# Kernel tuning notes

Measured on AMD Instinct MI355X. Metric: run time of the kernel, lower is better.

Reference implementation:

```python
import jax, jax.numpy as jnp
import numpy as np

B, S, D, H = 2, 2048, 1024, 16
HD = D // H  # head_dim = 64
ROPE_BASE = 10000.0
NEG_MIN = jnp.finfo(jnp.float32).min


def _rope_cos_sin(seq_len, head_dim):
    inv_freq = 1.0 / (ROPE_BASE ** (jnp.arange(0, head_dim, 2, dtype=jnp.float32) / head_dim))
    t = jnp.arange(seq_len, dtype=jnp.float32)
    freqs = jnp.einsum('i,j->ij', t, inv_freq)           # [S, HD/2]
    emb = jnp.concatenate([freqs, freqs], axis=-1)        # [S, HD]
    return jnp.cos(emb), jnp.sin(emb)


def _rotate_half(x):
    x1, x2 = jnp.split(x, 2, axis=-1)
    return jnp.concatenate([-x2, x1], axis=-1)


def setup_inputs() -> dict:
    key = jax.random.key(0)
    ks = jax.random.split(key, 5)
    sc = 0.02
    hidden_states = jax.random.normal(ks[0], (B, S, D), dtype=jnp.float32)
    wq = jax.random.normal(ks[1], (D, D), dtype=jnp.float32) * sc
    wk = jax.random.normal(ks[2], (D, D), dtype=jnp.float32) * sc
    wv = jax.random.normal(ks[3], (D, D), dtype=jnp.float32) * sc
    wo = jax.random.normal(ks[4], (D, D), dtype=jnp.float32) * sc
    # additive causal mask [B,1,S,S]: 0 on/below diagonal, large negative above
    causal = jnp.tril(jnp.ones((S, S), dtype=jnp.bool_))
    attention_mask = jnp.where(causal, 0.0, NEG_MIN)[None, None, :, :].astype(jnp.float32)
    attention_mask = jnp.broadcast_to(attention_mask, (B, 1, S, S))
    position_ids = jnp.broadcast_to(jnp.arange(S, dtype=jnp.int32)[None, :], (B, S))
    return {"hidden_states": hidden_states, "attention_mask": attention_mask,
            "wq": wq, "wk": wk, "wv": wv, "wo": wo, "position_ids": position_ids}


def reference(hidden_states, attention_mask, wq, wk, wv, wo, position_ids):
    bsz, q_len, _ = hidden_states.shape

    def shape_heads(x):
        return x.reshape(bsz, q_len, H, HD).transpose(0, 2, 1, 3)  # [B,H,S,HD]

    q = shape_heads(hidden_states @ wq)
    k = shape_heads(hidden_states @ wk)
    v = shape_heads(hidden_states @ wv)

    cos, sin = _rope_cos_sin(q_len, HD)                   # [S, HD]
    cos = cos[position_ids][:, None, :, :]                # [B,1,S,HD]
    sin = sin[position_ids][:, None, :, :]
    q = q * cos + _rotate_half(q) * sin
    k = k * cos + _rotate_half(k) * sin

    scores = jnp.einsum('bhqd,bhkd->bhqk', q, k) / jnp.sqrt(jnp.float32(HD))
    scores = jnp.maximum(scores + attention_mask, NEG_MIN)
    attn = jax.nn.softmax(scores, axis=-1)
    out = jnp.einsum('bhqk,bhkd->bhqd', attn, v)          # [B,H,S,HD]
    out = out.transpose(0, 2, 1, 3).reshape(bsz, q_len, D)
    return out @ wo
```

## Files before the change

kernel.cpp:

```cpp
#include <hip/hip_runtime.h>
#include <hip/hip_bf16.h>

#define B_ 2
#define S_ 2048
#define D_ 1024
#define H_ 16
#define HD_ 64

typedef unsigned short u16;
typedef __attribute__((ext_vector_type(8))) short short8;
typedef __attribute__((ext_vector_type(4))) float f32x4;

#if __has_builtin(__builtin_amdgcn_exp2f)
#define EXP2F(x) __builtin_amdgcn_exp2f(x)
#else
#define EXP2F(x) exp2f(x)
#endif

__device__ __forceinline__ u16 f2bf(float f) {
  union { float f; unsigned u; } v; v.f = f;
  unsigned r = v.u + 0x7fffu + ((v.u >> 16) & 1u);
  return (u16)(r >> 16);
}
__device__ __forceinline__ unsigned pkbf(float a, float b) {
  union { __hip_bfloat162 h; unsigned u; } v;
  v.h = __float22bfloat162_rn(float2{a, b});
  return v.u;
}
__device__ __forceinline__ void gload_lds16(const u16* g, u16* l) {
  __builtin_amdgcn_global_load_lds((const __attribute__((address_space(1))) void*)g,
                                   (__attribute__((address_space(3))) void*)l, 16, 0, 0);
}

__global__ __launch_bounds__(256) void prep_kernel(const float* __restrict__ hs,
                                                   const float* __restrict__ W0,
                                                   const float* __restrict__ W1,
                                                   const float* __restrict__ W2,
                                                   const float* __restrict__ W3,
                                                   u16* __restrict__ Xb,
                                                   u16* __restrict__ WT) {
  __shared__ float T[64][65];
  if (blockIdx.z == 4) {
    const int base = (blockIdx.y * 16 + blockIdx.x) * 4096 + threadIdx.x;
#pragma unroll 4
    for (int i = 0; i < 16; ++i) {
      const int idx = base + i * 256;
      const float4 v = ((const float4*)hs)[idx];
      ushort4 o;
      o.x = f2bf(v.x); o.y = f2bf(v.y); o.z = f2bf(v.z); o.w = f2bf(v.w);
      ((ushort4*)Xb)[idx] = o;
    }
    return;
  }
  const float* Wz[4] = {W0, W1, W2, W3};
  const float* W = Wz[blockIdx.z];
  u16* dst = WT + (size_t)blockIdx.z * (1024 * 1024);
  const int nb = blockIdx.x * 64, kb = blockIdx.y * 64;
  const int t = threadIdx.x;
  const int r = t >> 2, c4 = (t & 3) * 16;
#pragma unroll
  for (int i = 0; i < 4; ++i) {
    float4 v = *(const float4*)&W[(kb + r) * D_ + nb + c4 + i * 4];
    T[r][c4 + i * 4 + 0] = v.x;
    T[r][c4 + i * 4 + 1] = v.y;
    T[r][c4 + i * 4 + 2] = v.z;
    T[r][c4 + i * 4 + 3] = v.w;
  }
  __syncthreads();
#pragma unroll
  for (int i = 0; i < 4; ++i) {
    ushort4 o;
    o.x = f2bf(T[c4 + i * 4 + 0][r]);
    o.y = f2bf(T[c4 + i * 4 + 1][r]);
    o.z = f2bf(T[c4 + i * 4 + 2][r]);
    o.w = f2bf(T[c4 + i * 4 + 3][r]);
    *(ushort4*)&dst[(nb + r) * D_ + kb + c4 + i * 4] = o;
  }
}

template <int BN, int MODE, int DB>
__global__ __launch_bounds__(256) void gemm_kernel(const u16* __restrict__ A,
                                                   const u16* __restrict__ BT,
                                                   float* __restrict__ out0,
                                                   u16* __restrict__ oQ,
                                                   u16* __restrict__ oK,
                                                   u16* __restrict__ oV,
                                                   const int* __restrict__ posarr) {
  constexpr int K = D_;
  constexpr int NT = BN / 32;
  constexpr int BI = BN / 32;
  constexpr int ABANK = 128 * 64;
  constexpr int BBANK = BN * 64;
  constexpr int STAGE = (DB + 1) * (ABANK + BBANK);
  constexpr int EPIU = (MODE == 1) ? 128 * 136 : 0;
  constexpr int SMU = STAGE > EPIU ? STAGE : EPIU;
  __shared__ u16 smem[SMU];
  u16* AsP = smem;
  u16* BsP = smem + (DB + 1) * ABANK;

  const int t = threadIdx.x, lane = t & 63, w = t >> 6;
  const int l15 = lane & 15, quad = lane >> 4;
  const int n0 = blockIdx.x * BN, m0 = blockIdx.y * 128;
  const int wm = (w >> 1) * 64, wn = (w & 1) * (BN / 2);

  f32x4 acc[4][NT];
#pragma unroll
  for (int mt = 0; mt < 4; ++mt)
#pragma unroll
    for (int nt = 0; nt < NT; ++nt) acc[mt][nt] = (f32x4){0.f, 0.f, 0.f, 0.f};

  const u16* ag[4]; int aoff[4];
  const u16* bg[BI]; int boff[BI];
#pragma unroll
  for (int j = 0; j < 4; ++j) {
    int slot = w * 256 + j * 64 + lane;
    int row = slot >> 3, q = (slot & 7) ^ (row & 7);
    ag[j] = A + (size_t)(m0 + row) * K + q * 8;
    aoff[j] = (w * 256 + j * 64) * 8;
  }
#pragma unroll
  for (int j = 0; j < BI; ++j) {
    int slot = w * (BI * 64) + j * 64 + lane;
    int row = slot >> 3, q = (slot & 7) ^ (row & 7);
    bg[j] = BT + (size_t)(n0 + row) * K + q * 8;
    boff[j] = (w * (BI * 64) + j * 64) * 8;
  }

  auto stage = [&](int k0, int buf) {
#pragma unroll
    for (int j = 0; j < 4; ++j) gload_lds16(ag[j] + k0, AsP + buf * ABANK + aoff[j]);
#pragma unroll
    for (int j = 0; j < BI; ++j) gload_lds16(bg[j] + k0, BsP + buf * BBANK + boff[j]);
  };
  auto compute = [&](int buf) {
    const u16* Ab = AsP + buf * ABANK;
    const u16* Bb = BsP + buf * BBANK;
#pragma unroll
    for (int kc = 0; kc < 2; ++kc) {
      short8 af[4], bf[NT];
#pragma unroll
      for (int mt = 0; mt < 4; ++mt) {
        int row = wm + mt * 16 + l15;
        af[mt] = *(const short8*)&Ab[row * 64 + (((kc * 4 + quad) ^ (row & 7)) * 8)];
      }
#pragma unroll
      for (int nt = 0; nt < NT; ++nt) {
        int col = wn + nt * 16 + l15;
        bf[nt] = *(const short8*)&Bb[col * 64 + (((kc * 4 + quad) ^ (col & 7)) * 8)];
      }
#pragma unroll
      for (int mt = 0; mt < 4; ++mt)
#pragma unroll
        for (int nt = 0; nt < NT; ++nt)
          acc[mt][nt] = __builtin_amdgcn_mfma_f32_16x16x32_bf16(af[mt], bf[nt], acc[mt][nt], 0, 0, 0);
    }
  };

  if constexpr (DB == 0) {
    for (int k0 = 0; k0 < K; k0 += 64) {
      __syncthreads();
      stage(k0, 0);
      __syncthreads();
      compute(0);
    }
  } else {
    stage(0, 0);
#pragma unroll 1
    for (int it = 0; it < K / 64; ++it) {
      __syncthreads();
      if (it + 1 < K / 64) stage((it + 1) * 64, (it + 1) & 1);
      compute(it & 1);
    }
  }

  if (MODE == 0) {
#pragma unroll
    for (int mt = 0; mt < 4; ++mt) {
      const int row0 = m0 + wm + mt * 16 + quad * 4;
#pragma unroll
      for (int nt = 0; nt < NT; ++nt) {
        const int col = n0 + wn + nt * 16 + l15;
#pragma unroll
        for (int r = 0; r < 4; ++r) out0[(size_t)(row0 + r) * 1024 + col] = acc[mt][nt][r];
      }
    }
  } else {
    const int widx = n0 >> 10;
    if (widx == 2) {
      __syncthreads();
      u16* Epi = smem;
#pragma unroll
      for (int nt = 0; nt < NT; ++nt) {
        const int col = wn + nt * 16 + l15;
#pragma unroll
        for (int mt = 0; mt < 4; ++mt) {
          const int row0 = wm + mt * 16 + quad * 4;
          uint2 pk;
          pk.x = pkbf(acc[mt][nt][0], acc[mt][nt][1]);
          pk.y = pkbf(acc[mt][nt][2], acc[mt][nt][3]);
          *(uint2*)&Epi[col * 136 + row0] = pk;
        }
      }
      __syncthreads();
      const int col = t >> 1, half = t & 1;
      const int cc = (n0 + col) & 1023;
      const int h = cc >> 6, d = cc & 63;
      const int bb = m0 >> 11;
      const int s0 = (m0 & (S_ - 1)) + half * 64;
      u16* gp = oV + ((((size_t)(bb * H_ + h) * HD_ + d)) << 11) + s0;
#pragma unroll
      for (int i = 0; i < 8; ++i)
        ((uint4*)gp)[i] = *(const uint4*)&Epi[col * 136 + half * 64 + i * 8];
    } else {
      u16* dst = (widx == 0) ? oQ : oK;
      const float scale = (widx == 0) ? 0.18033688011f : 1.0f;
      float invf[2];
      invf[0] = exp2f(-0.41524101186f * (float)l15);
      invf[1] = exp2f(-0.41524101186f * (float)(16 + l15));
      const int h = ((n0 + wn) & 1023) >> 6;
#pragma unroll
      for (int mt = 0; mt < 4; ++mt) {
        const int row0 = m0 + wm + mt * 16 + quad * 4;
#pragma unroll
        for (int r = 0; r < 4; ++r) {
          const int rw = row0 + r;
          const int b = rw >> 11, s = rw & (S_ - 1);
          const float pos = (float)posarr[b * S_ + s];
          const size_t base = (((size_t)(b * H_ + h) * S_ + s) << 6);
#pragma unroll
          for (int nt2 = 0; nt2 < 2; ++nt2) {
            float sn, c;
            __sincosf(pos * invf[nt2], &sn, &c);
            const float x1 = acc[mt][nt2][r], x2 = acc[mt][nt2 + 2][r];
            const int d = nt2 * 16 + l15;
            dst[base + d] = f2bf((x1 * c - x2 * sn) * scale);
            dst[base + d + 32] = f2bf((x2 * c + x1 * sn) * scale);
          }
        }
      }
    }
  }
}

__global__ __launch_bounds__(256, 2) void attn_kernel(const u16* __restrict__ Q,
                                                      const u16* __restrict__ Kx,
                                                      const u16* __restrict__ Vt,
                                                      u16* __restrict__ AO) {
  __shared__ u16 Ks[2][2][512 * 8];
  __shared__ u16 Pw[4][128 * 8];
  const int t = threadIdx.x;
  const int lane = t & 63, w = t >> 6;
  const int l15 = lane & 15, quad = lane >> 4;
  const int idx = blockIdx.x;
  const int pr = (idx >> 3) & 15;
  const int bh = (idx & 7) | ((idx >> 7) << 3);
  const int qtA = pr, qtB = 31 - pr;
  const u16* qp = Q + bh * (S_ * HD_);
  const u16* kp = Kx + bh * (S_ * HD_);
  const u16* vp = Vt + bh * (HD_ * S_);
  const int wq16 = w * 16;
  const int q_loA = qtA * 64 + wq16;
  const int q_loB = qtB * 64 + wq16;

  int srow[2], sq[2];
#pragma unroll
  for (int jj = 0; jj < 2; ++jj) {
    int slot = w * 128 + jj * 64 + lane;
    srow[jj] = slot >> 3;
    sq[jj] = (slot & 7) ^ (srow[jj] & 7);
  }
  auto stageK = [&](int kt, u16* dst) {
#pragma unroll
    for (int jj = 0; jj < 2; ++jj)
      gload_lds16(kp + (size_t)(kt * 64 + srow[jj]) * 64 + sq[jj] * 8,
                  dst + (w * 128 + jj * 64) * 8);
  };
  auto stageGroup = [&](int g, int buf) {
    const int kt0 = g * 2;
    stageK(kt0, &Ks[buf][0][0]);
    if (kt0 + 1 <= qtB) stageK(kt0 + 1, &Ks[buf][1][0]);
  };
  auto loadKf = [&](int buf, int tt, short8* kf) {
#pragma unroll
    for (int kc = 0; kc < 2; ++kc)
#pragma unroll
      for (int nt = 0; nt < 4; ++nt) {
        const int row = nt * 16 + l15;
        kf[kc * 4 + nt] =
            *(const short8*)&Ks[buf][tt][(row * 8 + ((kc * 4 + quad) ^ (row & 7))) * 8];
      }
  };
  auto loadV = [&](int kt, short8* vf) {
#pragma unroll
    for (int dt = 0; dt < 4; ++dt)
#pragma unroll
      for (int kc = 0; kc < 2; ++kc)
        vf[dt * 2 + kc] =
            *(const short8*)&vp[(dt * 16 + l15) * S_ + kt * 64 + kc * 32 + quad * 8];
  };

  short8 qfA[2], qfB[2];
#pragma unroll
  for (int kc = 0; kc < 2; ++kc) {
    qfA[kc] = *(const short8*)&qp[(q_loA + l15) * HD_ + kc * 32 + quad * 8];
    qfB[kc] = *(const short8*)&qp[(q_loB + l15) * HD_ + kc * 32 + quad * 8];
  }

  f32x4 oA[4], oB[4];
  float mA = -INFINITY, lA = 0.f, mB = -INFINITY, lB = 0.f;
#pragma unroll
  for (int i = 0; i < 4; ++i) {
    oA[i] = (f32x4){0.f, 0.f, 0.f, 0.f};
    oB[i] = (f32x4){0.f, 0.f, 0.f, 0.f};
  }

  auto chainStep = [&](bool diag, const short8* qf, const short8* kf, const short8* vf,
                       f32x4* o, float& m_, float& l_) {
    f32x4 sa[4];
#pragma unroll
    for (int i = 0; i < 4; ++i) sa[i] = (f32x4){0.f, 0.f, 0.f, 0.f};
#pragma unroll
    for (int kc = 0; kc < 2; ++kc)
#pragma unroll
      for (int nt = 0; nt < 4; ++nt)
        sa[nt] = __builtin_amdgcn_mfma_f32_16x16x32_bf16(kf[kc * 4 + nt], qf[kc], sa[nt], 0, 0, 0);
    if (diag) {
#pragma unroll
      for (int nt = 0; nt < 4; ++nt)
#pragma unroll
        for (int r = 0; r < 4; ++r)
          if (nt * 16 + quad * 4 + r > wq16 + l15) sa[nt][r] = -INFINITY;
    }
    float mx = -INFINITY;
#pragma unroll
    for (int nt = 0; nt < 4; ++nt)
#pragma unroll
      for (int r = 0; r < 4; ++r) mx = fmaxf(mx, sa[nt][r]);
    mx = fmaxf(mx, __shfl_xor(mx, 16));
    mx = fmaxf(mx, __shfl_xor(mx, 32));
    const float mn = fmaxf(m_, mx);
    const float alpha = EXP2F(m_ - mn);
    m_ = mn;
    float p[16];
    float sum = 0.f;
#pragma unroll
    for (int nt = 0; nt < 4; ++nt)
#pragma unroll
      for (int r = 0; r < 4; ++r) {
        const float pe = EXP2F(sa[nt][r] - mn);
        p[nt * 4 + r] = pe;
        sum += pe;
      }
    sum += __shfl_xor(sum, 16);
    sum += __shfl_xor(sum, 32);
    l_ = l_ * alpha + sum;
#pragma unroll
    for (int dt = 0; dt < 4; ++dt)
#pragma unroll
      for (int r = 0; r < 4; ++r) o[dt][r] *= alpha;
#pragma unroll
    for (int nt = 0; nt < 4; ++nt) {
      const int q = nt * 2 + (quad >> 1);
      uint2 pk;
      pk.x = pkbf(p[nt * 4 + 0], p[nt * 4 + 1]);
      pk.y = pkbf(p[nt * 4 + 2], p[nt * 4 + 3]);
      *(uint2*)&Pw[w][(l15 * 8 + (q ^ (l15 & 7))) * 8 + (quad & 1) * 4] = pk;
    }
#pragma unroll
    for (int kc = 0; kc < 2; ++kc) {
      short8 pf = *(const short8*)&Pw[w][(l15 * 8 + (((kc * 4) + quad) ^ (l15 & 7))) * 8];
#pragma unroll
      for (int dt = 0; dt < 4; ++dt)
        o[dt] = __builtin_amdgcn_mfma_f32_16x16x32_bf16(vf[dt * 2 + kc], pf, o[dt], 0, 0, 0);
    }
  };

  const int ngroups = (qtB + 2) >> 1;
  short8 vf0[8], vf1[8], kf[8];
  stageGroup(0, 0);
  loadV(0, vf0);
#pragma unroll 1
  for (int g = 0; g < ngroups; ++g) {
    __syncthreads();
    if (g + 1 < ngroups) stageGroup(g + 1, (g + 1) & 1);
    const int buf = g & 1;
    const int kt0 = 2 * g;
    loadKf(buf, 0, kf);
    if (kt0 + 1 <= qtB) loadV(kt0 + 1, vf1);
    chainStep(kt0 == qtB, qfB, kf, vf0, oB, mB, lB);
    if (kt0 <= qtA) chainStep(kt0 == qtA, qfA, kf, vf0, oA, mA, lA);
    if (kt0 + 1 <= qtB) {
      loadKf(buf, 1, kf);
      if (kt0 + 2 <= qtB) loadV(kt0 + 2, vf0);
      chainStep(kt0 + 1 == qtB, qfB, kf, vf1, oB, mB, lB);
      if (kt0 + 1 <= qtA) chainStep(kt0 + 1 == qtA, qfA, kf, vf1, oA, mA, lA);
    }
  }

  const int b = bh >> 4, h = bh & 15;
  const float liA = 1.0f / lA, liB = 1.0f / lB;
  const size_t baseA = ((size_t)(b * S_ + q_loA + l15)) * D_ + h * HD_;
  const size_t baseB = ((size_t)(b * S_ + q_loB + l15)) * D_ + h * HD_;
#pragma unroll
  for (int dt = 0; dt < 4; ++dt)
#pragma unroll
    for (int rr = 0; rr < 2; ++rr) {
      *(unsigned*)&AO[baseA + dt * 16 + quad * 4 + rr * 2] =
          pkbf(oA[dt][rr * 2] * liA, oA[dt][rr * 2 + 1] * liA);
      *(unsigned*)&AO[baseB + dt * 16 + quad * 4 + rr * 2] =
          pkbf(oB[dt][rr * 2] * liB, oB[dt][rr * 2 + 1] * liB);
    }
}

extern "C" void kernel_launch(void* const* d_in, const int* in_sizes, int n_in,
                              void* d_out, int out_size, void* d_ws, size_t ws_size,
                              hipStream_t stream) {
  const float* hs = (const float*)d_in[0];
  const float* wq = (const float*)d_in[2];
  const float* wk = (const float*)d_in[3];
  const float* wv = (const float*)d_in[4];
  const float* wo = (const float*)d_in[5];
  const int* pos = (const int*)d_in[6];
  float* out = (float*)d_out;

  char* ws = (char*)d_ws;
  const size_t MB = (size_t)1 << 20;
  u16* Xb = (u16*)(ws);
  u16* WT = (u16*)(ws + 8 * MB);
  u16* Qh = (u16*)(ws + 16 * MB);
  u16* Kh = (u16*)(ws + 24 * MB);
  u16* Vt = (u16*)(ws + 32 * MB);
  u16* AO = (u16*)(ws + 40 * MB);

  prep_kernel<<<dim3(16, 16, 5), 256, 0, stream>>>(hs, wq, wk, wv, wo, Xb, WT);

  gemm_kernel<128, 1, 0><<<dim3(24, 32), 256, 0, stream>>>(Xb, WT, nullptr, Qh, Kh, Vt, pos);

  attn_kernel<<<512, 256, 0, stream>>>(Qh, Kh, Vt, AO);

  gemm_kernel<64, 0, 1><<<dim3(16, 32), 256, 0, stream>>>(AO, WT + 3 * 1024 * 1024, out,
                                                          nullptr, nullptr, nullptr, nullptr);
}
```

Before: 230.4 us.

## Stage V tiles through LDS and coalesce Q/K RoPE epilogue stores via shared memory

The attention kernel now loads V tiles into a swizzled LDS double buffer with async global-to-LDS copies alongside K, and walks one key tile per iteration instead of two. Before, V was read directly from global memory into registers. The QKV projection epilogue for Q and K now writes RoPE results into shared memory first and then emits 16-byte coalesced row stores per head, replacing scattered 2-byte global stores. This adds LDS traffic and extra barriers, halves the K staging per iteration, and removes the register prefetch of V that overlapped with compute.

New measurement: 210.4 us. 1.1x faster.

```diff
diff --git a/kernel.cpp b/kernel.cpp
--- a/kernel.cpp
+++ b/kernel.cpp
@@ -217,26 +217,37 @@
       float invf[2];
       invf[0] = exp2f(-0.41524101186f * (float)l15);
       invf[1] = exp2f(-0.41524101186f * (float)(16 + l15));
-      const int h = ((n0 + wn) & 1023) >> 6;
+      __syncthreads();
+      u16* Epi = smem;
 #pragma unroll
       for (int mt = 0; mt < 4; ++mt) {
-        const int row0 = m0 + wm + mt * 16 + quad * 4;
+        const int lrow0 = wm + mt * 16 + quad * 4;
 #pragma unroll
         for (int r = 0; r < 4; ++r) {
-          const int rw = row0 + r;
+          const int rw = m0 + lrow0 + r;
           const int b = rw >> 11, s = rw & (S_ - 1);
           const float pos = (float)posarr[b * S_ + s];
-          const size_t base = (((size_t)(b * H_ + h) * S_ + s) << 6);
 #pragma unroll
           for (int nt2 = 0; nt2 < 2; ++nt2) {
             float sn, c;
             __sincosf(pos * invf[nt2], &sn, &c);
             const float x1 = acc[mt][nt2][r], x2 = acc[mt][nt2 + 2][r];
             const int d = nt2 * 16 + l15;
-            dst[base + d] = f2bf((x1 * c - x2 * sn) * scale);
-            dst[base + d + 32] = f2bf((x2 * c + x1 * sn) * scale);
+            Epi[(lrow0 + r) * 136 + wn + d] = f2bf((x1 * c - x2 * sn) * scale);
+            Epi[(lrow0 + r) * 136 + wn + d + 32] = f2bf((x2 * c + x1 * sn) * scale);
           }
         }
+      }
+      __syncthreads();
+      const int bb = m0 >> 11, s0 = m0 & (S_ - 1);
+      const int sl = t >> 1, d0 = (t & 1) * 32;
+#pragma unroll
+      for (int hh = 0; hh < 2; ++hh) {
+        const int h = ((n0 + hh * 64) & 1023) >> 6;
+        u16* gp = dst + (((size_t)(bb * H_ + h) * S_ + s0 + sl) << 6) + d0;
+#pragma unroll
+        for (int k2 = 0; k2 < 4; ++k2)
+          ((uint4*)gp)[k2] = *(const uint4*)&Epi[sl * 136 + hh * 64 + d0 + k2 * 8];
       }
     }
   }
@@ -246,7 +257,8 @@
                                                       const u16* __restrict__ Kx,
                                                       const u16* __restrict__ Vt,
                                                       u16* __restrict__ AO) {
-  __shared__ u16 Ks[2][2][512 * 8];
+  __shared__ u16 Ks[2][512 * 8];
+  __shared__ u16 Vs[2][512 * 8];
   __shared__ u16 Pw[4][128 * 8];
   const int t = threadIdx.x;
   const int lane = t & 63, w = t >> 6;
@@ -269,34 +281,15 @@
     srow[jj] = slot >> 3;
     sq[jj] = (slot & 7) ^ (srow[jj] & 7);
   }
-  auto stageK = [&](int kt, u16* dst) {
+  auto stage = [&](int kt, int buf) {
 #pragma unroll
     for (int jj = 0; jj < 2; ++jj)
       gload_lds16(kp + (size_t)(kt * 64 + srow[jj]) * 64 + sq[jj] * 8,
-                  dst + (w * 128 + jj * 64) * 8);
-  };
-  auto stageGroup = [&](int g, int buf) {
-    const int kt0 = g * 2;
-    stageK(kt0, &Ks[buf][0][0]);
-    if (kt0 + 1 <= qtB) stageK(kt0 + 1, &Ks[buf][1][0]);
-  };
-  auto loadKf = [&](int buf, int tt, short8* kf) {
-#pragma unroll
-    for (int kc = 0; kc < 2; ++kc)
-#pragma unroll
-      for (int nt = 0; nt < 4; ++nt) {
-        const int row = nt * 16 + l15;
-        kf[kc * 4 + nt] =
-            *(const short8*)&Ks[buf][tt][(row * 8 + ((kc * 4 + quad) ^ (row & 7))) * 8];
-      }
-  };
-  auto loadV = [&](int kt, short8* vf) {
-#pragma unroll
-    for (int dt = 0; dt < 4; ++dt)
-#pragma unroll
-      for (int kc = 0; kc < 2; ++kc)
-        vf[dt * 2 + kc] =
-            *(const short8*)&vp[(dt * 16 + l15) * S_ + kt * 64 + kc * 32 + quad * 8];
+                  &Ks[buf][(w * 128 + jj * 64) * 8]);
+#pragma unroll
+    for (int jj = 0; jj < 2; ++jj)
+      gload_lds16(vp + (size_t)srow[jj] * S_ + kt * 64 + sq[jj] * 8,
+                  &Vs[buf][(w * 128 + jj * 64) * 8]);
   };
 
   short8 qfA[2], qfB[2];
@@ -375,26 +368,32 @@
     }
   };
 
-  const int ngroups = (qtB + 2) >> 1;
-  short8 vf0[8], vf1[8], kf[8];
-  stageGroup(0, 0);
-  loadV(0, vf0);
+  const int ktmax = qtB;
+  stage(0, 0);
 #pragma unroll 1
-  for (int g = 0; g < ngroups; ++g) {
+  for (int kt = 0; kt <= ktmax; ++kt) {
     __syncthreads();
-    if (g + 1 < ngroups) stageGroup(g + 1, (g + 1) & 1);
-    const int buf = g & 1;
-    const int kt0 = 2 * g;
-    loadKf(buf, 0, kf);
-    if (kt0 + 1 <= qtB) loadV(kt0 + 1, vf1);
-    chainStep(kt0 == qtB, qfB, kf, vf0, oB, mB, lB);
-    if (kt0 <= qtA) chainStep(kt0 == qtA, qfA, kf, vf0, oA, mA, lA);
-    if (kt0 + 1 <= qtB) {
-      loadKf(buf, 1, kf);
-      if (kt0 + 2 <= qtB) loadV(kt0 + 2, vf0);
-      chainStep(kt0 + 1 == qtB, qfB, kf, vf1, oB, mB, lB);
-      if (kt0 + 1 <= qtA) chainStep(kt0 + 1 == qtA, qfA, kf, vf1, oA, mA, lA);
-    }
+    if (kt < ktmax) stage(kt + 1, (kt + 1) & 1);
+    const int buf = kt & 1;
+    short8 kf[8], vf[8];
+#pragma unroll
+    for (int kc = 0; kc < 2; ++kc)
+#pragma unroll
+      for (int nt = 0; nt < 4; ++nt) {
+        const int row = nt * 16 + l15;
+        kf[kc * 4 + nt] =
+            *(const short8*)&Ks[buf][(row * 8 + ((kc * 4 + quad) ^ (row & 7))) * 8];
+      }
+#pragma unroll
+    for (int dt = 0; dt < 4; ++dt)
+#pragma unroll
+      for (int kc = 0; kc < 2; ++kc) {
+        const int row = dt * 16 + l15;
+        vf[dt * 2 + kc] =
+            *(const short8*)&Vs[buf][(row * 8 + ((kc * 4 + quad) ^ (row & 7))) * 8];
+      }
+    chainStep(kt == qtB, qfB, kf, vf, oB, mB, lB);
+    if (kt <= qtA) chainStep(kt == qtA, qfA, kf, vf, oA, mA, lA);
   }
 
   const int b = bh >> 4, h = bh & 15;
```
